# Performance work log

Hardware: AMD Instinct MI355X
Metric: run time of the kernel (lower is better)

## Reference

```python
import jax, jax.numpy as jnp
import numpy as np

B, H, W, C = 4, 56, 56, 128
HEADS, KS, DEPTH, DEPTH_CROSS = 4, 7, 2, 2
HID = 4 * C
EPS = 1e-5


def layer_norm(x, g, b):
    m = jnp.mean(x, axis=-1, keepdims=True)
    v = jnp.mean((x - m) ** 2, axis=-1, keepdims=True)
    return (x - m) * jax.lax.rsqrt(v + EPS) * g + b


def _nbr_idx(L, k):
    # clamped sliding-window start (NATTEN semantics)
    s = np.clip(np.arange(L) - k // 2, 0, L - k)
    n = s[:, None] + np.arange(k)            # [L,k] neighbor coords
    r = n - np.arange(L)[:, None] + (k - 1)  # [L,k] rpb index in [0, 2k-2]
    return jnp.asarray(n), jnp.asarray(r)


def neighborhood_attention(q, kx, vx, rpb):
    # q,kx,vx: [B,h,H,W,d]; rpb: [h,2k-1,2k-1]
    b, h, hh, ww, d = q.shape
    k = KS
    ni, ri = _nbr_idx(hh, k)
    nj, rj = _nbr_idx(ww, k)
    q = q * (d ** -0.5)

    def gather(t):
        t = jnp.take(t, ni.reshape(-1), axis=2).reshape(b, h, hh, k, ww, d)
        t = jnp.take(t, nj.reshape(-1), axis=4).reshape(b, h, hh, k, ww, k, d)
        return t.transpose(0, 1, 2, 4, 3, 5, 6)  # [B,h,H,W,k,k,d]

    kn = gather(kx)
    vn = gather(vx)
    attn = jnp.einsum('bnhwd,bnhwijd->bnhwij', q, kn)
    bias = rpb[:, ri][:, :, :, rj]          # [h,H,k,W,k]
    bias = bias.transpose(0, 1, 3, 2, 4)     # [h,H,W,k,k]
    attn = attn + bias[None]
    attn = jax.nn.softmax(attn.reshape(b, h, hh, ww, k * k), axis=-1)
    out = jnp.einsum('bnhwm,bnhwmd->bnhwd', attn,
                     vn.reshape(b, h, hh, ww, k * k, d))
    return out.transpose(0, 2, 3, 1, 4).reshape(b, hh, ww, h * d)


def mlp(x, f1w, f1b, f2w, f2b):
    return jax.nn.gelu(x @ f1w + f1b, approximate=False) @ f2w + f2b


def sa_layer(x, n1g, n1b, qkvw, qkvb, rpb, pw, pb, n2g, n2b, f1w, f1b, f2w, f2b):
    b, hh, ww, c = x.shape
    d = c // HEADS
    hn = layer_norm(x, n1g, n1b)
    qkv = (hn @ qkvw + qkvb).reshape(b, hh, ww, 3, HEADS, d).transpose(3, 0, 4, 1, 2, 5)
    a = neighborhood_attention(qkv[0], qkv[1], qkv[2], rpb) @ pw + pb
    x = x + a
    x = x + mlp(layer_norm(x, n2g, n2b), f1w, f1b, f2w, f2b)
    return x


def cross_layer(x_multi, q_in, n1g, n1b, qw, qb, kvw, kvb, rpb, pw, pb,
                n2g, n2b, f1w, f1b, f2w, f2b):
    b, hh, ww, c = x_multi.shape
    d = c // HEADS
    hn = layer_norm(x_multi, n1g, n1b)
    q = (q_in @ qw + qb).reshape(b, hh, ww, HEADS, d).transpose(0, 3, 1, 2, 4)
    kv = (hn @ kvw + kvb).reshape(b, hh, ww, 2, HEADS, d).transpose(3, 0, 4, 1, 2, 5)
    a = neighborhood_attention(q, kv[0], kv[1], rpb) @ pw + pb
    x = x_multi + a
    x = x + mlp(layer_norm(x, n2g, n2b), f1w, f1b, f2w, f2b)
    return x


def setup_inputs() -> dict:
    key = jax.random.key(0)
    ks = iter(jax.random.split(key, 64))

    def nrm(shape, s=0.02):
        return (jax.random.normal(next(ks), shape, dtype=jnp.float32) * s)

    D, Dc = DEPTH, DEPTH_CROSS
    inp = {
        'x': jax.random.normal(next(ks), (B, H, W, C), dtype=jnp.float32),
        'x_multi': jax.random.normal(next(ks), (B, H, W, C), dtype=jnp.float32),
        # self-attention NATLayers (stacked over depth)
        'sa_n1g': jnp.ones((D, C), jnp.float32), 'sa_n1b': jnp.zeros((D, C), jnp.float32),
        'sa_qkv_w': nrm((D, C, 3 * C)), 'sa_qkv_b': jnp.zeros((D, 3 * C), jnp.float32),
        'sa_rpb': nrm((D, HEADS, 2 * KS - 1, 2 * KS - 1)),
        'sa_proj_w': nrm((D, C, C)), 'sa_proj_b': jnp.zeros((D, C), jnp.float32),
        'sa_n2g': jnp.ones((D, C), jnp.float32), 'sa_n2b': jnp.zeros((D, C), jnp.float32),
        'sa_fc1_w': nrm((D, C, HID)), 'sa_fc1_b': jnp.zeros((D, HID), jnp.float32),
        'sa_fc2_w': nrm((D, HID, C)), 'sa_fc2_b': jnp.zeros((D, C), jnp.float32),
        # cross NATCrossLayers (stacked over depth_cross)
        'cr_n1g': jnp.ones((Dc, C), jnp.float32), 'cr_n1b': jnp.zeros((Dc, C), jnp.float32),
        'cr_q_w': nrm((Dc, C, C)), 'cr_q_b': jnp.zeros((Dc, C), jnp.float32),
        'cr_kv_w': nrm((Dc, C, 2 * C)), 'cr_kv_b': jnp.zeros((Dc, 2 * C), jnp.float32),
        'cr_rpb': nrm((Dc, HEADS, 2 * KS - 1, 2 * KS - 1)),
        'cr_proj_w': nrm((Dc, C, C)), 'cr_proj_b': jnp.zeros((Dc, C), jnp.float32),
        'cr_n2g': jnp.ones((Dc, C), jnp.float32), 'cr_n2b': jnp.zeros((Dc, C), jnp.float32),
        'cr_fc1_w': nrm((Dc, C, HID)), 'cr_fc1_b': jnp.zeros((Dc, HID), jnp.float32),
        'cr_fc2_w': nrm((Dc, HID, C)), 'cr_fc2_b': jnp.zeros((Dc, C), jnp.float32),
        # downsample: conv (2C -> 4C, 3x3, stride 2, no bias) + LayerNorm
        'ds_conv_w': nrm((3, 3, 2 * C, 4 * C)),
        'ds_ng': jnp.ones((4 * C,), jnp.float32), 'ds_nb': jnp.zeros((4 * C,), jnp.float32),
    }
    return inp


def reference(x, x_multi,
              sa_n1g, sa_n1b, sa_qkv_w, sa_qkv_b, sa_rpb, sa_proj_w, sa_proj_b,
              sa_n2g, sa_n2b, sa_fc1_w, sa_fc1_b, sa_fc2_w, sa_fc2_b,
              cr_n1g, cr_n1b, cr_q_w, cr_q_b, cr_kv_w, cr_kv_b, cr_rpb,
              cr_proj_w, cr_proj_b, cr_n2g, cr_n2b, cr_fc1_w, cr_fc1_b,
              cr_fc2_w, cr_fc2_b, ds_conv_w, ds_ng, ds_nb):
    x_cross = x
    for i in range(DEPTH):
        x = sa_layer(x, sa_n1g[i], sa_n1b[i], sa_qkv_w[i], sa_qkv_b[i], sa_rpb[i],
                     sa_proj_w[i], sa_proj_b[i], sa_n2g[i], sa_n2b[i],
                     sa_fc1_w[i], sa_fc1_b[i], sa_fc2_w[i], sa_fc2_b[i])
    for i in range(DEPTH_CROSS):
        x_cross = cross_layer(x_multi, x_cross, cr_n1g[i], cr_n1b[i], cr_q_w[i],
                              cr_q_b[i], cr_kv_w[i], cr_kv_b[i], cr_rpb[i],
                              cr_proj_w[i], cr_proj_b[i], cr_n2g[i], cr_n2b[i],
                              cr_fc1_w[i], cr_fc1_b[i], cr_fc2_w[i], cr_fc2_b[i])
    y = jnp.concatenate([x, x_cross], axis=-1)  # [B,H,W,2C]
    y = jax.lax.conv_general_dilated(y, ds_conv_w, (2, 2), [(1, 1), (1, 1)],
                                     dimension_numbers=('NHWC', 'HWIO', 'NHWC'))
    return layer_norm(y, ds_ng, ds_nb)  # [B,H/2,W/2,4C]
```

## Files before the change

kernel.cpp:

```cpp
#include <hip/hip_runtime.h>
#include <math.h>

#define NPIX 12544
#define CH   128
#define HEADS 4
#define HD   32
#define KS   7
#define HID  512
#define HH   56
#define WW   56

typedef __attribute__((ext_vector_type(8))) short bf16x8;
typedef __attribute__((ext_vector_type(4))) float f32x4;
typedef unsigned short u16;

__device__ inline float gelu_f(float x) { return 0.5f * x * (1.0f + erff(x * 0.70710678118654752f)); }

__device__ inline u16 rne_bf16(float x) {
    unsigned u = __float_as_uint(x);
    return (u16)((u + 0x7fffu + ((u >> 16) & 1u)) >> 16);
}
__device__ inline float bf2f(u16 u) {
    return __uint_as_float(((unsigned)u) << 16);
}


template<int BN, int MODE>
__device__ __forceinline__ void qln_body(char* sh,
    const float* __restrict__ Af, const u16* __restrict__ Bt,
    const float* __restrict__ lng, const float* __restrict__ lnb,
    const float* __restrict__ bias, u16* __restrict__ Cb,
    int N, int bx, int by)
{
    constexpr int NF = BN / 32;
    char* alsb = sh;
    char* blsb = sh + 16384;
    int t = threadIdx.x, lane = t & 63, w = t >> 6;
    int m0 = bx * 64, n0 = by * BN;
    int wr = w >> 1, wc = w & 1;

    {
        int rb = t >> 3, c8 = t & 7;
        float4 va[2][4];
        float sum[2], sq[2];
#pragma unroll
        for (int r2 = 0; r2 < 2; ++r2) {
            int row = r2 * 32 + rb;
            const float4* ap = reinterpret_cast<const float4*>(Af + (size_t)(m0 + row) * 128);
            va[r2][0] = ap[c8 * 2];
            va[r2][1] = ap[c8 * 2 + 1];
            va[r2][2] = ap[16 + c8 * 2];
            va[r2][3] = ap[16 + c8 * 2 + 1];
            float s = 0.f, q = 0.f;
#pragma unroll
            for (int e = 0; e < 4; ++e) {
                float4 x = va[r2][e];
                s += x.x + x.y + x.z + x.w;
                q += x.x * x.x + x.y * x.y + x.z * x.z + x.w * x.w;
            }
            sum[r2] = s; sq[r2] = q;
        }
#pragma unroll
        for (int o = 1; o < 8; o <<= 1) {
            sum[0] += __shfl_xor(sum[0], o); sq[0] += __shfl_xor(sq[0], o);
            sum[1] += __shfl_xor(sum[1], o); sq[1] += __shfl_xor(sq[1], o);
        }
        const float4* gp = reinterpret_cast<const float4*>(lng);
        const float4* bp = reinterpret_cast<const float4*>(lnb);
        float4 g[4], bb[4];
        g[0] = gp[c8 * 2];      g[1] = gp[c8 * 2 + 1];
        g[2] = gp[16 + c8 * 2]; g[3] = gp[16 + c8 * 2 + 1];
        bb[0] = bp[c8 * 2];      bb[1] = bp[c8 * 2 + 1];
        bb[2] = bp[16 + c8 * 2]; bb[3] = bp[16 + c8 * 2 + 1];
#pragma unroll
        for (int r2 = 0; r2 < 2; ++r2) {
            int row = r2 * 32 + rb;
            float mean = sum[r2] * (1.0f / 128.0f);
            float inv = rsqrtf(sq[r2] * (1.0f / 128.0f) - mean * mean + 1e-5f);
#pragma unroll
            for (int h = 0; h < 2; ++h) {
                float4 x0 = va[r2][h * 2], x1 = va[r2][h * 2 + 1];
                float4 g0 = g[h * 2], g1 = g[h * 2 + 1];
                float4 b0 = bb[h * 2], b1 = bb[h * 2 + 1];
                bf16x8 o;
                o[0] = (short)rne_bf16((x0.x - mean) * inv * g0.x + b0.x);
                o[1] = (short)rne_bf16((x0.y - mean) * inv * g0.y + b0.y);
                o[2] = (short)rne_bf16((x0.z - mean) * inv * g0.z + b0.z);
                o[3] = (short)rne_bf16((x0.w - mean) * inv * g0.w + b0.w);
                o[4] = (short)rne_bf16((x1.x - mean) * inv * g1.x + b1.x);
                o[5] = (short)rne_bf16((x1.y - mean) * inv * g1.y + b1.y);
                o[6] = (short)rne_bf16((x1.z - mean) * inv * g1.z + b1.z);
                o[7] = (short)rne_bf16((x1.w - mean) * inv * g1.w + b1.w);
                int byte = (h * 128 + c8 * 16) ^ ((row & 7) << 4);
                *reinterpret_cast<bf16x8*>(alsb + row * 256 + byte) = o;
            }
        }
    }

    f32x4 acc[2][NF] = {};
    for (int kk = 0; kk < 2; ++kk) {
#pragma unroll
        for (int i = 0; i < BN / 32; ++i) {
            int s = t + i * 256, row = s >> 3, ch = (s & 7) * 8;
            bf16x8 v = *reinterpret_cast<const bf16x8*>(Bt + (size_t)(n0 + row) * 128 + kk * 64 + ch);
            *reinterpret_cast<bf16x8*>(blsb + row * 128 + ((ch * 2) ^ ((row & 7) << 4))) = v;
        }
        __syncthreads();
#pragma unroll
        for (int sub = 0; sub < 2; ++sub) {
            int kba = (kk * 2 + sub) * 64 + (lane >> 4) * 16;
            int kbb = sub * 64 + (lane >> 4) * 16;
            bf16x8 af[2], bfr[NF];
#pragma unroll
            for (int mi = 0; mi < 2; ++mi) {
                int row = wr * 32 + mi * 16 + (lane & 15);
                af[mi] = *reinterpret_cast<const bf16x8*>(alsb + row * 256 + (kba ^ ((row & 7) << 4)));
            }
#pragma unroll
            for (int ni = 0; ni < NF; ++ni) {
                int row = wc * (BN / 2) + ni * 16 + (lane & 15);
                bfr[ni] = *reinterpret_cast<const bf16x8*>(blsb + row * 128 + (kbb ^ ((row & 7) << 4)));
            }
#pragma unroll
            for (int mi = 0; mi < 2; ++mi)
#pragma unroll
                for (int ni = 0; ni < NF; ++ni)
                    acc[mi][ni] = __builtin_amdgcn_mfma_f32_16x16x32_bf16(af[mi], bfr[ni], acc[mi][ni], 0, 0, 0);
        }
        __syncthreads();
    }

    int fq = lane >> 4, fr = lane & 15;
#pragma unroll
    for (int mi = 0; mi < 2; ++mi) {
#pragma unroll
        for (int ni = 0; ni < NF; ++ni) {
            int col = n0 + wc * (BN / 2) + ni * 16 + fr;
            float bv = bias[col];
#pragma unroll
            for (int j = 0; j < 4; ++j) {
                int row = m0 + wr * 32 + mi * 16 + fq * 4 + j;
                float v = acc[mi][ni][j] + bv;
                if constexpr (MODE == 1) {
                    Cb[(size_t)row * N + col] = rne_bf16(gelu_f(v));
                } else {
                    Cb[(size_t)row * N + col] = rne_bf16(v);
                }
            }
        }
    }
}

template<int MODE>
__device__ __forceinline__ void gemm_body(char* sh,
    const u16* __restrict__ A, const u16* __restrict__ Bt,
    const float* __restrict__ bias, const float* __restrict__ res,
    float* __restrict__ Cf, u16* __restrict__ Cb,
    int N, int K, int bx, int by)
{
    char* alsb = sh;
    char* blsb = sh + 4096;
    int t = threadIdx.x;
    int m0 = bx * 32, n0 = by * 64;
    int lane = t & 63, w = t >> 6;
    int wr = w >> 1, wc = w & 1;
    f32x4 acc[2] = {};
    for (int k0 = 0; k0 < K; k0 += 64) {
        {
            int s = t, row = s >> 3, ch = (s & 7) * 8;
            bf16x8 v = *reinterpret_cast<const bf16x8*>(A + (size_t)(m0 + row) * K + k0 + ch);
            *reinterpret_cast<bf16x8*>(alsb + row * 128 + ((ch * 2) ^ ((row & 7) << 4))) = v;
        }
#pragma unroll
        for (int i = 0; i < 2; ++i) {
            int s = t + i * 256, row = s >> 3, ch = (s & 7) * 8;
            bf16x8 v = *reinterpret_cast<const bf16x8*>(Bt + (size_t)(n0 + row) * K + k0 + ch);
            *reinterpret_cast<bf16x8*>(blsb + row * 128 + ((ch * 2) ^ ((row & 7) << 4))) = v;
        }
        __syncthreads();
#pragma unroll
        for (int kk = 0; kk < 2; ++kk) {
            int kb = kk * 64 + (lane >> 4) * 16;
            int row_a = wr * 16 + (lane & 15);
            bf16x8 af = *reinterpret_cast<const bf16x8*>(alsb + row_a * 128 + (kb ^ ((row_a & 7) << 4)));
#pragma unroll
            for (int ni = 0; ni < 2; ++ni) {
                int row = wc * 32 + ni * 16 + (lane & 15);
                bf16x8 bfr = *reinterpret_cast<const bf16x8*>(blsb + row * 128 + (kb ^ ((row & 7) << 4)));
                acc[ni] = __builtin_amdgcn_mfma_f32_16x16x32_bf16(af, bfr, acc[ni], 0, 0, 0);
            }
        }
        __syncthreads();
    }
    int fq = lane >> 4, fr = lane & 15;
#pragma unroll
    for (int ni = 0; ni < 2; ++ni) {
        int col = n0 + wc * 32 + ni * 16 + fr;
        float bv = bias[col];
#pragma unroll
        for (int j = 0; j < 4; ++j) {
            int row = m0 + wr * 16 + fq * 4 + j;
            float v = acc[ni][j] + bv;
            if constexpr (MODE == 2) {
                Cf[(size_t)row * N + col] = v + res[(size_t)row * N + col];
            } else if constexpr (MODE == 3) {
                Cb[(size_t)row * N + col] = rne_bf16(v);
            } else {
                float r2 = v + res[(size_t)row * N + col];
                Cf[(size_t)row * N + col] = r2;
                Cb[(size_t)row * N + col] = rne_bf16(r2);
            }
        }
    }
}


struct TDesc { const float* src; u16* dst; int K; int N; int tile0; };
struct TPack { TDesc d[19]; };

__global__ __launch_bounds__(256) void prep_kernel(TPack p, int ntile,
    const float* __restrict__ X, float* __restrict__ o1, float* __restrict__ o2,
    u16* __restrict__ ob, int n4)
{
    __shared__ float tl[32][33];
    if ((int)blockIdx.x < ntile) {
        int tile = blockIdx.x;
        int i = 0;
#pragma unroll 1
        while (i < 18 && tile >= p.d[i + 1].tile0) ++i;
        TDesc d = p.d[i];
        int local = tile - d.tile0;
        int ktiles = d.K >> 5;
        int lk = local % ktiles, ln_ = local / ktiles;
        int k0 = lk * 32, n0 = ln_ * 32;
        int tx = threadIdx.x & 31, ty = threadIdx.x >> 5;
#pragma unroll
        for (int r = 0; r < 4; ++r) {
            int row = ty * 4 + r;
            tl[row][tx] = d.src[(size_t)(k0 + row) * d.N + n0 + tx];
        }
        __syncthreads();
#pragma unroll
        for (int r = 0; r < 4; ++r) {
            int row = ty * 4 + r;
            d.dst[(size_t)(n0 + row) * d.K + k0 + tx] = rne_bf16(tl[tx][row]);
        }
    } else {
        int i = ((int)blockIdx.x - ntile) * 256 + threadIdx.x;
        if (i < n4) {
            float4 v = reinterpret_cast<const float4*>(X)[i];
            reinterpret_cast<float4*>(o1)[i] = v;
            reinterpret_cast<float4*>(o2)[i] = v;
            ushort4 o;
            o.x = rne_bf16(v.x); o.y = rne_bf16(v.y); o.z = rne_bf16(v.z); o.w = rne_bf16(v.w);
            reinterpret_cast<ushort4*>(ob)[i] = o;
        }
    }
}

__global__ __launch_bounds__(256) void stage1_kernel(
    const float* xb, const u16* qkvt, const float* n1g, const float* n1b, const float* qkvbias, u16* qkvout,
    const u16* xq, const u16* qwt, const float* qbias, u16* qout,
    const float* xm, const u16* kvt, const float* kn1g, const float* kn1b, const float* kvbias, u16* kvout)
{
    __shared__ __align__(16) char sh[32768];
    int b = blockIdx.x;
    if (b < 588) {
        qln_body<128, 3>(sh, xb, qkvt, n1g, n1b, qkvbias, qkvout, 384, b / 3, b % 3);
    } else if (b < 1372) {
        int lb = b - 588;
        gemm_body<3>(sh, xq, qwt, qbias, nullptr, nullptr, qout, 128, 128, lb >> 1, lb & 1);
    } else {
        int lb = b - 1372;
        qln_body<128, 3>(sh, xm, kvt, kn1g, kn1b, kvbias, kvout, 256, lb >> 1, lb & 1);
    }
}

__global__ __launch_bounds__(256) void proj_kernel(
    const u16* Asa, const u16* Bsa, const float* bsa, const float* rsa, float* Csa,
    const u16* Acr, const u16* Bcr, const float* bcr, const float* rcr, float* Ccr)
{
    __shared__ __align__(16) char sh[12288];
    if (blockIdx.x < 392)
        gemm_body<2>(sh, Asa, Bsa, bsa, rsa, Csa, nullptr, 128, 128, blockIdx.x, blockIdx.y);
    else
        gemm_body<2>(sh, Acr, Bcr, bcr, rcr, Ccr, nullptr, 128, 128, blockIdx.x - 392, blockIdx.y);
}

__global__ __launch_bounds__(256) void fc1_kernel(
    const float* Asa, const u16* Bsa, const float* g1, const float* b1, const float* bisa, u16* Csa,
    const float* Acr, const u16* Bcr, const float* g2, const float* b2, const float* bicr, u16* Ccr)
{
    __shared__ __align__(16) char sh[32768];
    if (blockIdx.x < 196)
        qln_body<128, 1>(sh, Asa, Bsa, g1, b1, bisa, Csa, 512, blockIdx.x, blockIdx.y);
    else
        qln_body<128, 1>(sh, Acr, Bcr, g2, b2, bicr, Ccr, 512, blockIdx.x - 196, blockIdx.y);
}

__global__ __launch_bounds__(256) void fc2_kernel(
    const u16* Asa, const u16* Bsa, const float* bsa, const float* rsa, float* Cfsa, u16* Cbsa,
    const u16* Acr, const u16* Bcr, const float* bcr, const float* rcr, float* Cfcr, u16* Cbcr)
{
    __shared__ __align__(16) char sh[12288];
    if (blockIdx.x < 392)
        gemm_body<4>(sh, Asa, Bsa, bsa, rsa, Cfsa, Cbsa, 128, 512, blockIdx.x, blockIdx.y);
    else
        gemm_body<4>(sh, Acr, Bcr, bcr, rcr, Cfcr, Cbcr, 128, 512, blockIdx.x - 392, blockIdx.y);
}

__global__ __launch_bounds__(256) void conv_mfma_kernel(
    const u16* __restrict__ Xb, const u16* __restrict__ Xc,
    const u16* __restrict__ Wt, float* __restrict__ Out)
{
    __shared__ u16 Als[32 * 64];
    __shared__ u16 Bls[64 * 64];
    char* alsb = reinterpret_cast<char*>(Als);
    char* blsb = reinterpret_cast<char*>(Bls);
    int t = threadIdx.x;
    int m0 = blockIdx.x * 32, n0 = blockIdx.y * 64;
    int lane = t & 63, w = t >> 6, wr = w >> 1, wc = w & 1;

    int arow = t >> 3, ach = (t & 7) * 8;
    int pm = m0 + arow;
    int b = pm / 784; int rem = pm - b * 784;
    int oi = rem / 28, oj = rem - oi * 28;
    int pb = b * 56, ib = 2 * oi - 1, jb = 2 * oj - 1;

    f32x4 acc[2] = {};
    for (int k0 = 0; k0 < 2304; k0 += 64) {
        {
            int k = k0 + ach;
            int tap = k >> 8, c = k & 255;
            int ky = (tap * 11) >> 5, kx = tap - ky * 3;
            int ii = ib + ky, jj = jb + kx;
            bf16x8 v = {};
            if ((unsigned)ii < 56u && (unsigned)jj < 56u) {
                const u16* src = (c < 128) ? Xb : Xc;
                v = *reinterpret_cast<const bf16x8*>(src + (size_t)((pb + ii) * 56 + jj) * 128 + (c & 127));
            }
            *reinterpret_cast<bf16x8*>(alsb + arow * 128 + ((ach * 2) ^ ((arow & 7) << 4))) = v;
        }
#pragma unroll
        for (int i = 0; i < 2; ++i) {
            int s = t + i * 256, row = s >> 3, ch = (s & 7) * 8;
            bf16x8 v = *reinterpret_cast<const bf16x8*>(Wt + (size_t)(n0 + row) * 2304 + k0 + ch);
            *reinterpret_cast<bf16x8*>(blsb + row * 128 + ((ch * 2) ^ ((row & 7) << 4))) = v;
        }
        __syncthreads();
#pragma unroll
        for (int kk = 0; kk < 2; ++kk) {
            int kb = kk * 64 + (lane >> 4) * 16;
            int row_a = wr * 16 + (lane & 15);
            bf16x8 af = *reinterpret_cast<const bf16x8*>(alsb + row_a * 128 + (kb ^ ((row_a & 7) << 4)));
#pragma unroll
            for (int ni = 0; ni < 2; ++ni) {
                int row = wc * 32 + ni * 16 + (lane & 15);
                bf16x8 bfr = *reinterpret_cast<const bf16x8*>(blsb + row * 128 + (kb ^ ((row & 7) << 4)));
                acc[ni] = __builtin_amdgcn_mfma_f32_16x16x32_bf16(af, bfr, acc[ni], 0, 0, 0);
            }
        }
        __syncthreads();
    }
    int fq = lane >> 4, fr = lane & 15;
#pragma unroll
    for (int ni = 0; ni < 2; ++ni) {
        int col = n0 + wc * 32 + ni * 16 + fr;
#pragma unroll
        for (int j = 0; j < 4; ++j) {
            int row = m0 + wr * 16 + fq * 4 + j;
            Out[(size_t)row * 512 + col] = acc[ni][j];
        }
    }
}

__global__ __launch_bounds__(256) void na2_kernel(
    const u16* __restrict__ Qa, int qlda, const u16* __restrict__ Ka, const u16* __restrict__ Va,
    int kvlda, const float* __restrict__ rpba, u16* __restrict__ Outa,
    const u16* __restrict__ Qb, int qldb, const u16* __restrict__ Kb, const u16* __restrict__ Vb,
    int kvldb, const float* __restrict__ rpbb, u16* __restrict__ Outb)
{
    __shared__ u16 KSls[144 * 40];
    __shared__ u16 Pls[32 * 160];
    __shared__ u16 Vtls[32 * 160];
    u16* Kls = KSls;
    u16* Sls16 = KSls;
    float* rls = reinterpret_cast<float*>(KSls + 4864);

    int sel = blockIdx.y >> 2;
    const u16* Q  = sel ? Qb : Qa;     int qld  = sel ? qldb : qlda;
    const u16* Kx = sel ? Kb : Ka;     const u16* Vx = sel ? Vb : Va;
    int kvld = sel ? kvldb : kvlda;
    const float* rpb = sel ? rpbb : rpba;
    u16* Out = sel ? Outb : Outa;
    int h = blockIdx.y & 3;

    int t = threadIdx.x, lane = t & 63, w = t >> 6;
    int blk = blockIdx.x;
    int b = blk / 98; int rem = blk - b * 98;
    int ti = rem / 7, tj = rem - ti * 7;
    int i0 = ti * 4, j0 = tj * 8;
    int r0 = min(max(i0 - 3, 0), 46), c0 = min(max(j0 - 3, 0), 42);
    int gbase = (b * 56 + r0) * 56 + c0;

    bf16x8 aq[2];
#pragma unroll
    for (int qt = 0; qt < 2; ++qt) {
        int q = qt * 16 + (lane & 15);
        int qi = q >> 3, qj = q & 7;
        aq[qt] = *reinterpret_cast<const bf16x8*>(
            Q + (size_t)((b * 56 + i0 + qi) * 56 + j0 + qj) * qld + h * 32 + (lane >> 4) * 8);
    }

    {
        uint4 z4 = make_uint4(0, 0, 0, 0);
        for (int i = t; i < 640; i += 256) reinterpret_cast<uint4*>(Pls)[i] = z4;
        if (t < 160) {
            int r = t / 5, k = t - r * 5;
            ushort4 z2; z2.x = 0; z2.y = 0; z2.z = 0; z2.w = 0;
            *reinterpret_cast<ushort4*>(Vtls + r * 160 + 140 + k * 4) = z2;
        }
    }

    for (int idx = t; idx < 280; idx += 256) {
        int pr2 = idx >> 2, c8 = (idx & 3) * 8;
        int p0 = pr2 * 2, p1 = p0 + 1;
        int ur0 = p0 / 14, uc0 = p0 - ur0 * 14;
        int ur1 = p1 / 14, uc1 = p1 - ur1 * 14;
        size_t g0 = (size_t)(gbase + ur0 * 56 + uc0) * kvld + h * 32 + c8;
        size_t g1 = (size_t)(gbase + ur1 * 56 + uc1) * kvld + h * 32 + c8;
        *reinterpret_cast<bf16x8*>(Kls + p0 * 40 + c8) = *reinterpret_cast<const bf16x8*>(Kx + g0);
        *reinterpret_cast<bf16x8*>(Kls + p1 * 40 + c8) = *reinterpret_cast<const bf16x8*>(Kx + g1);
        bf16x8 v0 = *reinterpret_cast<const bf16x8*>(Vx + g0);
        bf16x8 v1 = *reinterpret_cast<const bf16x8*>(Vx + g1);
#pragma unroll
        for (int e = 0; e < 8; ++e) {
            ushort2 pr; pr.x = (u16)v0[e]; pr.y = (u16)v1[e];
            *reinterpret_cast<ushort2*>(Vtls + (c8 + e) * 160 + p0) = pr;
        }
    }
    if (t < 16) {
        int r = 140 + (t >> 2), c8 = (t & 3) * 8;
        bf16x8 z8 = {};
        *reinterpret_cast<bf16x8*>(Kls + r * 40 + c8) = z8;
    }
    __syncthreads();

    f32x4 sacc[3][2] = {};
#pragma unroll
    for (int pi = 0; pi < 3; ++pi) {
        int pt = w + pi * 4;
        if (pt < 9) {
            bf16x8 bfrag = *reinterpret_cast<const bf16x8*>(Kls + (pt * 16 + (lane & 15)) * 40 + (lane >> 4) * 8);
#pragma unroll
            for (int qt = 0; qt < 2; ++qt)
                sacc[pi][qt] = __builtin_amdgcn_mfma_f32_16x16x32_bf16(aq[qt], bfrag, sacc[pi][qt], 0, 0, 0);
        }
    }
    __syncthreads();
#pragma unroll
    for (int pi = 0; pi < 3; ++pi) {
        int pt = w + pi * 4;
        if (pt < 9) {
#pragma unroll
            for (int qt = 0; qt < 2; ++qt) {
                int p = pt * 16 + (lane & 15), qr = qt * 16 + (lane >> 4) * 4;
#pragma unroll
                for (int j = 0; j < 4; ++j) Sls16[(qr + j) * 152 + p] = rne_bf16(sacc[pi][qt][j]);
            }
        }
    }
    if (t < 169) rls[t] = rpb[h * 169 + t];
    __syncthreads();

    int ai = lane / 7, aj = lane - ai * 7;
    for (int qq = 0; qq < 8; ++qq) {
        int q = w * 8 + qq;
        int qi = q >> 3, qj = q & 7;
        int i = i0 + qi, j = j0 + qj;
        int si = min(max(i - 3, 0), 49), sj = min(max(j - 3, 0), 49);
        int pu_base = (si - r0) * 14 + (sj - c0);
        float s = -1e30f; int pu = 0;
        if (lane < 49) {
            pu = pu_base + ai * 14 + aj;
            s = bf2f(Sls16[q * 152 + pu]) * 0.17677669529663687f
              + rls[(si - i + 6 + ai) * 13 + (sj - j + 6 + aj)];
        }
        float m = s;
#pragma unroll
        for (int o = 32; o > 0; o >>= 1) m = fmaxf(m, __shfl_xor(m, o));
        float e = (lane < 49) ? expf(s - m) : 0.f;
        float sum = e;
#pragma unroll
        for (int o = 32; o > 0; o >>= 1) sum += __shfl_xor(sum, o);
        if (lane < 49) Pls[q * 160 + pu] = rne_bf16(e / sum);
    }
    __syncthreads();

    int qt = w >> 1, ct = w & 1;
    f32x4 oacc = {};
#pragma unroll
    for (int k = 0; k < 5; ++k) {
        bf16x8 pa = *reinterpret_cast<const bf16x8*>(Pls + (qt * 16 + (lane & 15)) * 160 + k * 32 + (lane >> 4) * 8);
        bf16x8 vb = *reinterpret_cast<const bf16x8*>(Vtls + (ct * 16 + (lane & 15)) * 160 + k * 32 + (lane >> 4) * 8);
        oacc = __builtin_amdgcn_mfma_f32_16x16x32_bf16(pa, vb, oacc, 0, 0, 0);
    }
    int ch = ct * 16 + (lane & 15);
#pragma unroll
    for (int j = 0; j < 4; ++j) {
        int q = qt * 16 + (lane >> 4) * 4 + j;
        int qi = q >> 3, qj = q & 7;
        Out[(size_t)((b * 56 + i0 + qi) * 56 + j0 + qj) * CH + h * 32 + ch] = rne_bf16(oacc[j]);
    }
}

__global__ __launch_bounds__(256) void ln512_out_kernel(const float* __restrict__ in,
    const float* __restrict__ g, const float* __restrict__ b, float* __restrict__ out)
{
    int w = threadIdx.x >> 6, lane = threadIdx.x & 63;
    int p = blockIdx.x * 4 + w;
    const float4* ip = reinterpret_cast<const float4*>(in + (size_t)p * 512);
    float4 v0 = ip[lane * 2], v1 = ip[lane * 2 + 1];
    float vals[8] = { v0.x, v0.y, v0.z, v0.w, v1.x, v1.y, v1.z, v1.w };
    float s = 0.f, sq = 0.f;
#pragma unroll
    for (int q = 0; q < 8; ++q) { s += vals[q]; sq += vals[q] * vals[q]; }
#pragma unroll
    for (int o = 32; o > 0; o >>= 1) { s += __shfl_xor(s, o); sq += __shfl_xor(sq, o); }
    float mean = s * (1.0f / 512.0f);
    float inv = rsqrtf(sq * (1.0f / 512.0f) - mean * mean + 1e-5f);
#pragma unroll
    for (int q = 0; q < 8; ++q) {
        int c = lane * 8 + q;
        out[(size_t)p * 512 + c] = (vals[q] - mean) * inv * g[c] + b[c];
    }
}

extern "C" void kernel_launch(void* const* d_in, const int* in_sizes, int n_in,
                              void* d_out, int out_size, void* d_ws, size_t ws_size,
                              hipStream_t stream)
{
    const float* X      = (const float*)d_in[0];
    const float* XM     = (const float*)d_in[1];
    const float* sa_n1g = (const float*)d_in[2];
    const float* sa_n1b = (const float*)d_in[3];
    const float* sa_qkvw= (const float*)d_in[4];
    const float* sa_qkvb= (const float*)d_in[5];
    const float* sa_rpb = (const float*)d_in[6];
    const float* sa_pw  = (const float*)d_in[7];
    const float* sa_pb  = (const float*)d_in[8];
    const float* sa_n2g = (const float*)d_in[9];
    const float* sa_n2b = (const float*)d_in[10];
    const float* sa_f1w = (const float*)d_in[11];
    const float* sa_f1b = (const float*)d_in[12];
    const float* sa_f2w = (const float*)d_in[13];
    const float* sa_f2b = (const float*)d_in[14];
    const float* cr_n1g = (const float*)d_in[15];
    const float* cr_n1b = (const float*)d_in[16];
    const float* cr_qw  = (const float*)d_in[17];
    const float* cr_qb  = (const float*)d_in[18];
    const float* cr_kvw = (const float*)d_in[19];
    const float* cr_kvb = (const float*)d_in[20];
    const float* cr_rpb = (const float*)d_in[21];
    const float* cr_pw  = (const float*)d_in[22];
    const float* cr_pb  = (const float*)d_in[23];
    const float* cr_n2g = (const float*)d_in[24];
    const float* cr_n2b = (const float*)d_in[25];
    const float* cr_f1w = (const float*)d_in[26];
    const float* cr_f1b = (const float*)d_in[27];
    const float* cr_f2w = (const float*)d_in[28];
    const float* cr_f2b = (const float*)d_in[29];
    const float* dconvw = (const float*)d_in[30];
    const float* ds_ng  = (const float*)d_in[31];
    const float* ds_nb  = (const float*)d_in[32];

    const size_t NC = (size_t)NPIX * CH;
    float* ws   = (float*)d_ws;
    float* xb   = ws;
    float* xcb  = xb + NC;
    float* bigR = xcb + NC;
    u16* bigb   = (u16*)bigR;
    u16* hnb    = (u16*)(bigR + 2 * NC);
    u16* attnb  = hnb + NC;
    u16* xcbbf  = attnb + NC;
    u16* xbbf   = xcbbf + NC;
    u16* qkvb   = xbbf + NC;
    u16* bufQb  = qkvb + (size_t)NPIX * 384;
    u16* wa     = bufQb + NC;
    u16* kvb    = bigb;
    u16* bigcr  = qkvb;

    TPack tp;
    int tile = 0, idx = 0;
    u16* p = wa;
    u16* qkvt[2]; u16* pwt[2]; u16* f1t[2]; u16* f2t[2];
    u16* qt[2];   u16* kvt[2]; u16* cpt[2]; u16* cf1t[2];
    u16* cf2t[2]; u16* convt;
    auto add = [&](const float* s, u16*& dst, int K, int N) {
        dst = p;
        tp.d[idx].src = s; tp.d[idx].dst = p; tp.d[idx].K = K; tp.d[idx].N = N; tp.d[idx].tile0 = tile;
        tile += (K / 32) * (N / 32); p += (size_t)K * N; ++idx;
    };
    for (int l = 0; l < 2; ++l) add(sa_qkvw + (size_t)l * 128 * 384, qkvt[l], 128, 384);
    for (int l = 0; l < 2; ++l) add(sa_pw   + (size_t)l * 128 * 128, pwt[l],  128, 128);
    for (int l = 0; l < 2; ++l) add(sa_f1w  + (size_t)l * 128 * 512, f1t[l],  128, 512);
    for (int l = 0; l < 2; ++l) add(sa_f2w  + (size_t)l * 512 * 128, f2t[l],  512, 128);
    for (int l = 0; l < 2; ++l) add(cr_qw   + (size_t)l * 128 * 128, qt[l],   128, 128);
    for (int l = 0; l < 2; ++l) add(cr_kvw  + (size_t)l * 128 * 256, kvt[l],  128, 256);
    for (int l = 0; l < 2; ++l) add(cr_pw   + (size_t)l * 128 * 128, cpt[l],  128, 128);
    for (int l = 0; l < 2; ++l) add(cr_f1w  + (size_t)l * 128 * 512, cf1t[l], 128, 512);
    for (int l = 0; l < 2; ++l) add(cr_f2w  + (size_t)l * 512 * 128, cf2t[l], 512, 128);
    add(dconvw, convt, 2304, 512);

    const int n4 = NPIX * CH / 4;
    const int ndup = (n4 + 255) / 256;
    prep_kernel<<<tile + ndup, 256, 0, stream>>>(tp, tile, X, xb, xcb, xcbbf, n4);

    for (int l = 0; l < 2; ++l) {
        stage1_kernel<<<1764, 256, 0, stream>>>(
            xb, qkvt[l], sa_n1g + l * CH, sa_n1b + l * CH, sa_qkvb + l * 384, qkvb,
            xcbbf, qt[l], cr_qb + l * CH, bufQb,
            XM, kvt[l], cr_n1g + l * CH, cr_n1b + l * CH, cr_kvb + l * 256, kvb);
        na2_kernel<<<dim3(392, 8), 256, 0, stream>>>(
            qkvb, 384, qkvb + 128, qkvb + 256, 384, sa_rpb + l * HEADS * 169, attnb,
            bufQb, 128, kvb, kvb + 128, 256, cr_rpb + l * HEADS * 169, hnb);
        proj_kernel<<<dim3(784, 2), 256, 0, stream>>>(
            attnb, pwt[l], sa_pb + l * CH, xb, xb,
            hnb, cpt[l], cr_pb + l * CH, XM, xcb);
        fc1_kernel<<<dim3(392, 4), 256, 0, stream>>>(
            xb, f1t[l], sa_n2g + l * CH, sa_n2b + l * CH, sa_f1b + l * HID, bigb,
            xcb, cf1t[l], cr_n2g + l * CH, cr_n2b + l * CH, cr_f1b + l * HID, bigcr);
        fc2_kernel<<<dim3(784, 2), 256, 0, stream>>>(
            bigb, f2t[l], sa_f2b + l * CH, xb, xb, xbbf,
            bigcr, cf2t[l], cr_f2b + l * CH, xcb, xcb, xcbbf);
    }

    conv_mfma_kernel<<<dim3(3136 / 32, 512 / 64), 256, 0, stream>>>(xbbf, xcbbf, convt, bigR);
    ln512_out_kernel<<<3136 / 4, 256, 0, stream>>>(bigR, ds_ng, ds_nb, (float*)d_out);
}
```

Before: 215.9 us.

## Give fc2 full-width 32x128 tiles and drop redundant fp32 copy of input

Replaces the generic gemm_body for the fc2 GEMM (K=512, N=128) with a dedicated body in which each block computes a 32x128 output tile across four waves, each wave doing 2x2 MFMA tiles. This halves the grid and loads each A row panel once instead of twice across N-blocks. Separately, the prep kernel no longer writes a second fp32 copy of X into the cross-branch buffer, saving one full-tensor store. The larger tile uses more LDS (20 KB) and leaves fewer blocks to spread across the CUs.

```diff
diff --git a/kernel.cpp b/kernel.cpp
--- a/kernel.cpp
+++ b/kernel.cpp
@@ -203,12 +203,71 @@
             float v = acc[ni][j] + bv;
             if constexpr (MODE == 2) {
                 Cf[(size_t)row * N + col] = v + res[(size_t)row * N + col];
-            } else if constexpr (MODE == 3) {
+            } else {
                 Cb[(size_t)row * N + col] = rne_bf16(v);
-            } else {
-                float r2 = v + res[(size_t)row * N + col];
-                Cf[(size_t)row * N + col] = r2;
-                Cb[(size_t)row * N + col] = rne_bf16(r2);
+            }
+        }
+    }
+}
+
+__device__ __forceinline__ void fc2_body(char* sh,
+    const u16* __restrict__ A, const u16* __restrict__ Bt,
+    const float* __restrict__ bias, const float* __restrict__ res,
+    float* __restrict__ Cf, u16* __restrict__ Cb, int bx)
+{
+    char* alsb = sh;
+    char* blsb = sh + 4096;
+    int t = threadIdx.x, lane = t & 63, w = t >> 6;
+    int m0 = bx * 32;
+    f32x4 acc[2][2] = {};
+    for (int k0 = 0; k0 < 512; k0 += 64) {
+        {
+            int row = t >> 3, ch = (t & 7) * 8;
+            bf16x8 v = *reinterpret_cast<const bf16x8*>(A + (size_t)(m0 + row) * 512 + k0 + ch);
+            *reinterpret_cast<bf16x8*>(alsb + row * 128 + ((ch * 2) ^ ((row & 7) << 4))) = v;
+        }
+#pragma unroll
+        for (int i = 0; i < 4; ++i) {
+            int s = t + i * 256, row = s >> 3, ch = (s & 7) * 8;
+            bf16x8 v = *reinterpret_cast<const bf16x8*>(Bt + (size_t)row * 512 + k0 + ch);
+            *reinterpret_cast<bf16x8*>(blsb + row * 128 + ((ch * 2) ^ ((row & 7) << 4))) = v;
+        }
+        __syncthreads();
+#pragma unroll
+        for (int kk = 0; kk < 2; ++kk) {
+            int kb = kk * 64 + (lane >> 4) * 16;
+            bf16x8 af[2], bfr[2];
+#pragma unroll
+            for (int mi = 0; mi < 2; ++mi) {
+                int row_a = mi * 16 + (lane & 15);
+                af[mi] = *reinterpret_cast<const bf16x8*>(alsb + row_a * 128 + (kb ^ ((row_a & 7) << 4)));
+            }
+#pragma unroll
+            for (int ni = 0; ni < 2; ++ni) {
+                int row = w * 32 + ni * 16 + (lane & 15);
+                bfr[ni] = *reinterpret_cast<const bf16x8*>(blsb + row * 128 + (kb ^ ((row & 7) << 4)));
+            }
+#pragma unroll
+            for (int mi = 0; mi < 2; ++mi)
+#pragma unroll
+                for (int ni = 0; ni < 2; ++ni)
+                    acc[mi][ni] = __builtin_amdgcn_mfma_f32_16x16x32_bf16(af[mi], bfr[ni], acc[mi][ni], 0, 0, 0);
+        }
+        __syncthreads();
+    }
+    int fq = lane >> 4, fr = lane & 15;
+#pragma unroll
+    for (int mi = 0; mi < 2; ++mi) {
+#pragma unroll
+        for (int ni = 0; ni < 2; ++ni) {
+            int col = w * 32 + ni * 16 + fr;
+            float bv = bias[col];
+#pragma unroll
+            for (int j = 0; j < 4; ++j) {
+                int row = m0 + mi * 16 + fq * 4 + j;
+                float r2 = acc[mi][ni][j] + bv + res[(size_t)row * 128 + col];
+                Cf[(size_t)row * 128 + col] = r2;
+                Cb[(size_t)row * 128 + col] = rne_bf16(r2);
             }
         }
     }
@@ -219,7 +278,7 @@
 struct TPack { TDesc d[19]; };
 
 __global__ __launch_bounds__(256) void prep_kernel(TPack p, int ntile,
-    const float* __restrict__ X, float* __restrict__ o1, float* __restrict__ o2,
+    const float* __restrict__ X, float* __restrict__ o1,
     u16* __restrict__ ob, int n4)
 {
     __shared__ float tl[32][33];
@@ -250,7 +309,6 @@
         if (i < n4) {
             float4 v = reinterpret_cast<const float4*>(X)[i];
             reinterpret_cast<float4*>(o1)[i] = v;
-            reinterpret_cast<float4*>(o2)[i] = v;
             ushort4 o;
             o.x = rne_bf16(v.x); o.y = rne_bf16(v.y); o.z = rne_bf16(v.z); o.w = rne_bf16(v.w);
             reinterpret_cast<ushort4*>(ob)[i] = o;
@@ -302,11 +360,11 @@
     const u16* Asa, const u16* Bsa, const float* bsa, const float* rsa, float* Cfsa, u16* Cbsa,
     const u16* Acr, const u16* Bcr, const float* bcr, const float* rcr, float* Cfcr, u16* Cbcr)
 {
-    __shared__ __align__(16) char sh[12288];
+    __shared__ __align__(16) char sh[20480];
     if (blockIdx.x < 392)
-        gemm_body<4>(sh, Asa, Bsa, bsa, rsa, Cfsa, Cbsa, 128, 512, blockIdx.x, blockIdx.y);
+        fc2_body(sh, Asa, Bsa, bsa, rsa, Cfsa, Cbsa, blockIdx.x);
     else
-        gemm_body<4>(sh, Acr, Bcr, bcr, rcr, Cfcr, Cbcr, 128, 512, blockIdx.x - 392, blockIdx.y);
+        fc2_body(sh, Acr, Bcr, bcr, rcr, Cfcr, Cbcr, blockIdx.x - 392);
 }
 
 __global__ __launch_bounds__(256) void conv_mfma_kernel(
@@ -614,7 +672,7 @@
 
     const int n4 = NPIX * CH / 4;
     const int ndup = (n4 + 255) / 256;
-    prep_kernel<<<tile + ndup, 256, 0, stream>>>(tp, tile, X, xb, xcb, xcbbf, n4);
+    prep_kernel<<<tile + ndup, 256, 0, stream>>>(tp, tile, X, xb, xcbbf, n4);
 
     for (int l = 0; l < 2; ++l) {
         stage1_kernel<<<1764, 256, 0, stream>>>(
@@ -630,7 +688,7 @@
         fc1_kernel<<<dim3(392, 4), 256, 0, stream>>>(
             xb, f1t[l], sa_n2g + l * CH, sa_n2b + l * CH, sa_f1b + l * HID, bigb,
             xcb, cf1t[l], cr_n2g + l * CH, cr_n2b + l * CH, cr_f1b + l * HID, bigcr);
-        fc2_kernel<<<dim3(784, 2), 256, 0, stream>>>(
+        fc2_kernel<<<784, 256, 0, stream>>>(
             bigb, f2t[l], sa_f2b + l * CH, xb, xb, xbbf,
             bigcr, cf2t[l], cr_f2b + l * CH, xcb, xcb, xcbbf);
     }
```

After: 219.2 us. Within noise of the previous version (+1.5%).
